# Kernel tuning notes

Measured on AMD Instinct MI355X. Metric: run time of the kernel, lower is better.

## Reference

```python
import jax, jax.numpy as jnp
import numpy as np

B, T, N, P2, K_S = 8, 64, 128, 256, 64

def setup_inputs() -> dict:
    key = jax.random.key(0)
    k1, k2, k3, k4 = jax.random.split(key, 4)
    x = jax.random.normal(k1, (B, T, N, P2), dtype=jnp.float32)
    W_Q = jax.random.uniform(k2, (P2, K_S), dtype=jnp.float32)
    W_K = jax.random.uniform(k3, (P2, K_S), dtype=jnp.float32)
    W_V = jax.random.uniform(k4, (P2, P2), dtype=jnp.float32)
    return {"x": x, "W_Q": W_Q, "W_K": W_K, "W_V": W_V}

def reference(x, W_Q, W_K, W_V):
    # x: [B, T, N, P2]
    q = jnp.einsum('btnp,pk->btnk', x, W_Q)          # [B,T,N,K_S]
    k = jnp.einsum('btnp,pk->btnk', x, W_K)          # [B,T,N,K_S]
    v = jnp.einsum('btnp,pq->btnq', x, W_V)          # [B,T,N,P2]
    scale = jnp.sqrt(jnp.asarray(K_S, dtype=x.dtype))
    scores = jnp.einsum('btik,btjk->btij', q, k) / scale  # [B,T,N,N]
    # NOTE: original uses nn.Softmax(dim=1) -> softmax over the T axis.
    attn = jax.nn.softmax(scores, axis=1)
    return jnp.einsum('btij,btjq->btiq', attn, v)    # [B,T,N,P2]
```

## Files before the change

kernel.cpp:

```cpp
#include <hip/hip_runtime.h>
#include <hip/hip_bf16.h>

#define Bv 8
#define Tv 64
#define Nv 128
#define P2v 256
#define KSv 64

typedef __attribute__((ext_vector_type(8))) short bf8;
typedef __attribute__((ext_vector_type(4))) float f4;

#define MFMA16(a, b, c) __builtin_amdgcn_mfma_f32_16x16x32_bf16((a), (b), (c), 0, 0, 0)

__device__ __forceinline__ unsigned short f2bf(float f) {
  unsigned u = __float_as_uint(f);
  return (unsigned short)((u + 0x7fffu + ((u >> 16) & 1u)) >> 16);
}
__device__ __forceinline__ float bf2f(unsigned short h) {
  return __uint_as_float(((unsigned)h) << 16);
}

__device__ __forceinline__ int swz64(int r, int c) {
  return r * 64 + ((((c >> 3)) ^ (r & 7)) << 3) + (c & 7);
}
__device__ __forceinline__ int swz32(int r, int c) {
  return r * 32 + ((((c >> 3)) ^ (r & 3)) << 3) + (c & 7);
}
__device__ __forceinline__ int swz128(int r, int c) {
  return r * 128 + ((((c >> 3)) ^ (r & 7)) << 3) + (c & 7);
}

__global__ __launch_bounds__(256) void prep_w_kernel(
    const float* __restrict__ Wq, const float* __restrict__ Wk,
    const float* __restrict__ Wv, unsigned short* __restrict__ wqh,
    unsigned short* __restrict__ wql, unsigned short* __restrict__ wkh,
    unsigned short* __restrict__ wkl, unsigned short* __restrict__ wvf) {
  const int e = blockIdx.x * 256 + threadIdx.x;
  if (e < 32768) {
    const float* W = (e < 16384) ? Wq : Wk;
    unsigned short* oh = (e < 16384) ? wqh : wkh;
    unsigned short* ol = (e < 16384) ? wql : wkl;
    const int t = e & 16383;
    const int jj = t & 7, lane = (t >> 3) & 63, nt = (t >> 9) & 3, pt = t >> 11;
    const int p = pt * 32 + 8 * (lane >> 4) + jj;
    const int n = nt * 16 + (lane & 15);
    const float v = W[p * KSv + n];
    const unsigned short h = f2bf(v);
    oh[t] = h;
    ol[t] = f2bf(v - bf2f(h));
  } else {
    const int t = e - 32768;
    const int jj = t & 7, lane = (t >> 3) & 63, nt = (t >> 9) & 15, pt = t >> 13;
    const int p = pt * 32 + 8 * (lane >> 4) + jj;
    const int q = nt * 16 + (lane & 15);
    wvf[t] = f2bf(Wv[p * P2v + q]);
  }
}

__global__ __launch_bounds__(512) void qk_kernel(
    const float* __restrict__ x, const unsigned short* __restrict__ wqh,
    const unsigned short* __restrict__ wql,
    const unsigned short* __restrict__ wkh,
    const unsigned short* __restrict__ wkl, float* __restrict__ S,
    unsigned short* __restrict__ Xh) {
  __shared__ alignas(16) unsigned short xh_l[Nv * 32];
  __shared__ alignas(16) unsigned short xl_l[Nv * 32];
  __shared__ alignas(16) unsigned short qh_l[Nv * KSv];
  __shared__ alignas(16) unsigned short ql_l[Nv * KSv];
  __shared__ alignas(16) unsigned short kh_l[Nv * KSv];
  __shared__ alignas(16) unsigned short kl_l[Nv * KSv];
  const int bt = blockIdx.x;
  const float* __restrict__ X = x + (size_t)bt * (Nv * P2v);
  const int tid = threadIdx.x, lane = tid & 63, wid = tid >> 6;
  const int lg = lane >> 4, lr = lane & 15;
  const bool isQ = (wid < 4);
  const int nt = wid & 3;
  const unsigned short* __restrict__ wh = isQ ? wqh : wkh;
  const unsigned short* __restrict__ wl = isQ ? wql : wkl;

  const f4 zero = {0.f, 0.f, 0.f, 0.f};
  f4 acc[8];
#pragma unroll
  for (int rt = 0; rt < 8; ++rt) acc[rt] = zero;

  const int srow = tid >> 2;
  const int sp = (tid & 3) * 8;
  const float* __restrict__ Xrow = X + srow * P2v + sp;
  unsigned short* __restrict__ XhRow =
      Xh ? (Xh + (size_t)(bt * Nv + srow) * P2v + sp) : (unsigned short*)0;

  float4 pv0 = *(const float4*)(Xrow);
  float4 pv1 = *(const float4*)(Xrow + 4);
  bf8 pwh = *(const bf8*)(wh + (nt * 64 + lane) * 8);
  bf8 pwl = *(const bf8*)(wl + (nt * 64 + lane) * 8);

  for (int c = 0; c < 8; ++c) {
    ushort4 h0, l0, h1, l1;
    h0.x = f2bf(pv0.x); l0.x = f2bf(pv0.x - bf2f(h0.x));
    h0.y = f2bf(pv0.y); l0.y = f2bf(pv0.y - bf2f(h0.y));
    h0.z = f2bf(pv0.z); l0.z = f2bf(pv0.z - bf2f(h0.z));
    h0.w = f2bf(pv0.w); l0.w = f2bf(pv0.w - bf2f(h0.w));
    h1.x = f2bf(pv1.x); l1.x = f2bf(pv1.x - bf2f(h1.x));
    h1.y = f2bf(pv1.y); l1.y = f2bf(pv1.y - bf2f(h1.y));
    h1.z = f2bf(pv1.z); l1.z = f2bf(pv1.z - bf2f(h1.z));
    h1.w = f2bf(pv1.w); l1.w = f2bf(pv1.w - bf2f(h1.w));
    const bf8 cwh = pwh, cwl = pwl;

    if (XhRow) {
      *(ushort4*)(XhRow + c * 32) = h0;
      *(ushort4*)(XhRow + c * 32 + 4) = h1;
    }

    __syncthreads();
    const int off = swz32(srow, sp);
    *(ushort4*)(xh_l + off) = h0;
    *(ushort4*)(xh_l + off + 4) = h1;
    *(ushort4*)(xl_l + off) = l0;
    *(ushort4*)(xl_l + off + 4) = l1;

    if (c < 7) {
      pv0 = *(const float4*)(Xrow + (c + 1) * 32);
      pv1 = *(const float4*)(Xrow + (c + 1) * 32 + 4);
      const int wo = (((c + 1) * 4 + nt) * 64 + lane) * 8;
      pwh = *(const bf8*)(wh + wo);
      pwl = *(const bf8*)(wl + wo);
    }
    __syncthreads();
#pragma unroll
    for (int rt = 0; rt < 8; ++rt) {
      const int xoff = swz32(rt * 16 + lr, lg * 8);
      const bf8 xh = *(const bf8*)(xh_l + xoff);
      const bf8 xl = *(const bf8*)(xl_l + xoff);
      acc[rt] = MFMA16(xh, cwh, acc[rt]);
      acc[rt] = MFMA16(xh, cwl, acc[rt]);
      acc[rt] = MFMA16(xl, cwh, acc[rt]);
    }
  }

  unsigned short* const oh = isQ ? qh_l : kh_l;
  unsigned short* const ol = isQ ? ql_l : kl_l;
#pragma unroll
  for (int rt = 0; rt < 8; ++rt) {
#pragma unroll
    for (int rr = 0; rr < 4; ++rr) {
      const int i = rt * 16 + 4 * lg + rr;
      const int ks = nt * 16 + lr;
      const int off = swz64(i, ks);
      const float v = acc[rt][rr];
      const unsigned short h = f2bf(v);
      oh[off] = h;
      ol[off] = f2bf(v - bf2f(h));
    }
  }
  __syncthreads();

  const int r0 = wid * 16;
  f4 aS[8];
#pragma unroll
  for (int n = 0; n < 8; ++n) aS[n] = zero;
#pragma unroll
  for (int kt2 = 0; kt2 < 2; ++kt2) {
    const int qoff = swz64(r0 + lr, kt2 * 32 + lg * 8);
    const bf8 fqh = *(const bf8*)(qh_l + qoff);
    const bf8 fql = *(const bf8*)(ql_l + qoff);
#pragma unroll
    for (int n = 0; n < 8; ++n) {
      const int koff = swz64(n * 16 + lr, kt2 * 32 + lg * 8);
      const bf8 fkh = *(const bf8*)(kh_l + koff);
      const bf8 fkl = *(const bf8*)(kl_l + koff);
      aS[n] = MFMA16(fqh, fkh, aS[n]);
      aS[n] = MFMA16(fqh, fkl, aS[n]);
      aS[n] = MFMA16(fql, fkh, aS[n]);
    }
  }
  float* __restrict__ Sb = S + (size_t)bt * (Nv * Nv);
#pragma unroll
  for (int n = 0; n < 8; ++n) {
#pragma unroll
    for (int rr = 0; rr < 4; ++rr) {
      Sb[(r0 + 4 * lg + rr) * Nv + n * 16 + lr] = aS[n][rr] * 0.125f;
    }
  }
}

__global__ __launch_bounds__(256) void softmax_t_kernel(
    const float* __restrict__ S, unsigned short* __restrict__ Abf) {
  const int idx = blockIdx.x * 256 + threadIdx.x;
  const int j = idx & (Nv - 1);
  const int i = (idx >> 7) & (Nv - 1);
  const int b = idx >> 14;
  const size_t base = ((size_t)b * Tv * Nv * Nv) + (size_t)i * Nv + j;

  float vals[Tv];
  float m = -1e30f;
#pragma unroll
  for (int t = 0; t < Tv; ++t) {
    const float v = S[base + (size_t)t * Nv * Nv];
    vals[t] = v;
    m = fmaxf(m, v);
  }
  float s = 0.f;
#pragma unroll
  for (int t = 0; t < Tv; ++t) {
    const float e = __expf(vals[t] - m);
    vals[t] = e;
    s += e;
  }
  const float inv = 1.f / s;
#pragma unroll
  for (int t = 0; t < Tv; ++t) {
    Abf[base + (size_t)t * Nv * Nv] = f2bf(vals[t] * inv);
  }
}

__global__ __launch_bounds__(512) void av_direct_kernel(
    const unsigned short* __restrict__ Xh,
    const unsigned short* __restrict__ wvf,
    const unsigned short* __restrict__ Abf, float* __restrict__ out) {
  __shared__ alignas(16) unsigned short vth[Nv * Nv];
  const int bt = blockIdx.x;
  const unsigned short* __restrict__ Xb = Xh + (size_t)bt * (Nv * P2v);
  const unsigned short* __restrict__ Ab = Abf + (size_t)bt * (Nv * Nv);
  float* __restrict__ ob = out + (size_t)bt * (Nv * P2v);
  const int tid = threadIdx.x, lane = tid & 63, wid = tid >> 6;
  const int lg = lane >> 4, lr = lane & 15;
  const int r0 = wid * 16;

  const f4 zero = {0.f, 0.f, 0.f, 0.f};
  f4 aV[16];
#pragma unroll
  for (int n = 0; n < 16; ++n) aV[n] = zero;

#pragma unroll
  for (int kt = 0; kt < 8; ++kt) {
    const bf8 fv0 = *(const bf8*)(wvf + ((kt * 16 + wid) * 64 + lane) * 8);
    const bf8 fv1 = *(const bf8*)(wvf + ((kt * 16 + 8 + wid) * 64 + lane) * 8);
#pragma unroll
    for (int rt = 0; rt < 8; ++rt) {
      const bf8 xf = *(const bf8*)(Xb + (rt * 16 + lr) * P2v + kt * 32 + lg * 8);
      aV[rt] = MFMA16(xf, fv0, aV[rt]);
      aV[8 + rt] = MFMA16(xf, fv1, aV[8 + rt]);
    }
  }

  bf8 af[4];
#pragma unroll
  for (int kt = 0; kt < 4; ++kt) {
    af[kt] = *(const bf8*)(Ab + (r0 + lr) * Nv + kt * 32 + lg * 8);
  }

#pragma unroll
  for (int h = 0; h < 2; ++h) {
    if (h == 1) __syncthreads();
    const int ql = wid * 16 + lr;
#pragma unroll
    for (int rt = 0; rt < 8; ++rt) {
      const int j0 = rt * 16 + 4 * lg;
      ushort4 pk;
      pk.x = f2bf(aV[h * 8 + rt][0]);
      pk.y = f2bf(aV[h * 8 + rt][1]);
      pk.z = f2bf(aV[h * 8 + rt][2]);
      pk.w = f2bf(aV[h * 8 + rt][3]);
      *(ushort4*)(vth + swz128(ql, j0)) = pk;
    }
    __syncthreads();

    f4 aO[8];
#pragma unroll
    for (int n = 0; n < 8; ++n) aO[n] = zero;
#pragma unroll
    for (int kt = 0; kt < 4; ++kt) {
#pragma unroll
      for (int n = 0; n < 8; ++n) {
        const bf8 vf =
            *(const bf8*)(vth + swz128(n * 16 + lr, kt * 32 + lg * 8));
        aO[n] = MFMA16(af[kt], vf, aO[n]);
      }
    }
#pragma unroll
    for (int n = 0; n < 8; ++n) {
#pragma unroll
      for (int rr = 0; rr < 4; ++rr) {
        ob[(r0 + 4 * lg + rr) * P2v + h * 128 + n * 16 + lr] = aO[n][rr];
      }
    }
  }
}

__global__ __launch_bounds__(512) void av_kernel(
    const float* __restrict__ x, const unsigned short* __restrict__ wvf,
    const unsigned short* __restrict__ Abf, float* __restrict__ out) {
  __shared__ alignas(16) unsigned short xa[Nv * KSv];
  __shared__ alignas(16) unsigned short vth[Nv * Nv];
  const int bt = blockIdx.x;
  const float* __restrict__ X = x + (size_t)bt * (Nv * P2v);
  const unsigned short* __restrict__ Ab = Abf + (size_t)bt * (Nv * Nv);
  float* __restrict__ ob = out + (size_t)bt * (Nv * P2v);
  const int tid = threadIdx.x, lane = tid & 63, wid = tid >> 6;
  const int lg = lane >> 4, lr = lane & 15;
  const int r0 = wid * 16;

  bf8 af[4];
#pragma unroll
  for (int kt = 0; kt < 4; ++kt) {
    af[kt] = *(const bf8*)(Ab + (r0 + lr) * Nv + kt * 32 + lg * 8);
  }

  const f4 zero = {0.f, 0.f, 0.f, 0.f};
  f4 aV[16];
#pragma unroll
  for (int n = 0; n < 16; ++n) aV[n] = zero;

  const int srow = tid >> 4;
  const int sp = (tid & 15) * 4;
  const float* __restrict__ Xrow = X + srow * P2v + sp;

  float4 pf0 = *(const float4*)(Xrow);
  float4 pf1 = *(const float4*)(Xrow + 32 * P2v);
  float4 pf2 = *(const float4*)(Xrow + 64 * P2v);
  float4 pf3 = *(const float4*)(Xrow + 96 * P2v);

  for (int c = 0; c < 4; ++c) {
    ushort4 q0, q1, q2, q3;
    q0.x = f2bf(pf0.x); q0.y = f2bf(pf0.y); q0.z = f2bf(pf0.z); q0.w = f2bf(pf0.w);
    q1.x = f2bf(pf1.x); q1.y = f2bf(pf1.y); q1.z = f2bf(pf1.z); q1.w = f2bf(pf1.w);
    q2.x = f2bf(pf2.x); q2.y = f2bf(pf2.y); q2.z = f2bf(pf2.z); q2.w = f2bf(pf2.w);
    q3.x = f2bf(pf3.x); q3.y = f2bf(pf3.y); q3.z = f2bf(pf3.z); q3.w = f2bf(pf3.w);

    __syncthreads();
    *(ushort4*)(xa + swz64(srow, sp)) = q0;
    *(ushort4*)(xa + swz64(srow + 32, sp)) = q1;
    *(ushort4*)(xa + swz64(srow + 64, sp)) = q2;
    *(ushort4*)(xa + swz64(srow + 96, sp)) = q3;

    if (c < 3) {
      pf0 = *(const float4*)(Xrow + (c + 1) * 64);
      pf1 = *(const float4*)(Xrow + (c + 1) * 64 + 32 * P2v);
      pf2 = *(const float4*)(Xrow + (c + 1) * 64 + 64 * P2v);
      pf3 = *(const float4*)(Xrow + (c + 1) * 64 + 96 * P2v);
    }
    __syncthreads();
#pragma unroll
    for (int ktl = 0; ktl < 2; ++ktl) {
      const int kt = c * 2 + ktl;
#pragma unroll
      for (int h = 0; h < 2; ++h) {
        const int ntile = h * 8 + wid;
        const int o = ((kt * 16 + ntile) * 64 + lane) * 8;
        const bf8 fv = *(const bf8*)(wvf + o);
#pragma unroll
        for (int rt = 0; rt < 8; ++rt) {
          const bf8 xh =
              *(const bf8*)(xa + swz64(rt * 16 + lr, ktl * 32 + lg * 8));
          aV[h * 8 + rt] = MFMA16(xh, fv, aV[h * 8 + rt]);
        }
      }
    }
  }

#pragma unroll
  for (int h = 0; h < 2; ++h) {
    if (h == 1) __syncthreads();
    const int ql = wid * 16 + lr;
#pragma unroll
    for (int rt = 0; rt < 8; ++rt) {
      const int j0 = rt * 16 + 4 * lg;
      ushort4 pk;
      pk.x = f2bf(aV[h * 8 + rt][0]);
      pk.y = f2bf(aV[h * 8 + rt][1]);
      pk.z = f2bf(aV[h * 8 + rt][2]);
      pk.w = f2bf(aV[h * 8 + rt][3]);
      *(ushort4*)(vth + swz128(ql, j0)) = pk;
    }
    __syncthreads();

    f4 aO[8];
#pragma unroll
    for (int n = 0; n < 8; ++n) aO[n] = zero;
#pragma unroll
    for (int kt = 0; kt < 4; ++kt) {
#pragma unroll
      for (int n = 0; n < 8; ++n) {
        const bf8 vf =
            *(const bf8*)(vth + swz128(n * 16 + lr, kt * 32 + lg * 8));
        aO[n] = MFMA16(af[kt], vf, aO[n]);
      }
    }
#pragma unroll
    for (int n = 0; n < 8; ++n) {
#pragma unroll
      for (int rr = 0; rr < 4; ++rr) {
        ob[(r0 + 4 * lg + rr) * P2v + h * 128 + n * 16 + lr] = aO[n][rr];
      }
    }
  }
}

extern "C" void kernel_launch(void* const* d_in, const int* in_sizes, int n_in,
                              void* d_out, int out_size, void* d_ws,
                              size_t ws_size, hipStream_t stream) {
  const float* x = (const float*)d_in[0];
  const float* Wq = (const float*)d_in[1];
  const float* Wk = (const float*)d_in[2];
  const float* Wv = (const float*)d_in[3];
  float* out = (float*)d_out;

  unsigned short* wqh = (unsigned short*)d_ws;
  unsigned short* wql = wqh + 16384;
  unsigned short* wkh = wql + 16384;
  unsigned short* wkl = wkh + 16384;
  unsigned short* wvf = wkl + 16384;
  float* S = (float*)((char*)d_ws + 262144);
  unsigned short* Abf = (unsigned short*)((char*)d_ws + 262144 + 33554432);
  unsigned short* Xh =
      (unsigned short*)((char*)d_ws + 262144 + 33554432 + 16777216);
  const size_t need_big = 262144ull + 33554432ull + 16777216ull + 33554432ull;
  const bool big = (ws_size >= need_big);

  hipLaunchKernelGGL(prep_w_kernel, dim3(384), dim3(256), 0, stream, Wq, Wk,
                     Wv, wqh, wql, wkh, wkl, wvf);
  hipLaunchKernelGGL(qk_kernel, dim3(Bv * Tv), dim3(512), 0, stream, x, wqh,
                     wql, wkh, wkl, S, big ? Xh : (unsigned short*)0);
  hipLaunchKernelGGL(softmax_t_kernel, dim3(Bv * Nv * Nv / 256), dim3(256), 0,
                     stream, S, Abf);
  if (big) {
    hipLaunchKernelGGL(av_direct_kernel, dim3(Bv * Tv), dim3(512), 0, stream,
                       Xh, wvf, Abf, out);
  } else {
    hipLaunchKernelGGL(av_kernel, dim3(Bv * Tv), dim3(512), 0, stream, x, wvf,
                       Abf, out);
  }
}
```

Before: 97.32 us.

## Alias LDS buffers, stage X through LDS in AV kernel, vectorize score/output stores

The QK kernel now aliases its x-staging and q/k LDS buffers into a single array, which lowers LDS use per block and may allow higher occupancy. The S and output stores are vectorized to float4 by swapping the MFMA operands so each lane holds contiguous columns. The direct AV kernel now stages bf16 X tiles in swizzled LDS with register prefetch instead of reading fragments straight from global memory. The V^T buffer is split into two 64-column swizzled halves. These changes add extra barriers and depend on the aliasing being safe after the added sync.

After: 82.17 us. -15.6%, faster.

```diff
diff --git a/kernel.cpp b/kernel.cpp
--- a/kernel.cpp
+++ b/kernel.cpp
@@ -25,9 +25,6 @@
 }
 __device__ __forceinline__ int swz32(int r, int c) {
   return r * 32 + ((((c >> 3)) ^ (r & 3)) << 3) + (c & 7);
-}
-__device__ __forceinline__ int swz128(int r, int c) {
-  return r * 128 + ((((c >> 3)) ^ (r & 7)) << 3) + (c & 7);
 }
 
 __global__ __launch_bounds__(256) void prep_w_kernel(
@@ -63,12 +60,13 @@
     const unsigned short* __restrict__ wkh,
     const unsigned short* __restrict__ wkl, float* __restrict__ S,
     unsigned short* __restrict__ Xh) {
-  __shared__ alignas(16) unsigned short xh_l[Nv * 32];
-  __shared__ alignas(16) unsigned short xl_l[Nv * 32];
-  __shared__ alignas(16) unsigned short qh_l[Nv * KSv];
-  __shared__ alignas(16) unsigned short ql_l[Nv * KSv];
-  __shared__ alignas(16) unsigned short kh_l[Nv * KSv];
-  __shared__ alignas(16) unsigned short kl_l[Nv * KSv];
+  __shared__ alignas(16) unsigned short sh[4 * Nv * KSv];
+  unsigned short* const xh_l = sh;
+  unsigned short* const xl_l = sh + Nv * 32;
+  unsigned short* const qh_l = sh;
+  unsigned short* const ql_l = sh + 8192;
+  unsigned short* const kh_l = sh + 16384;
+  unsigned short* const kl_l = sh + 24576;
   const int bt = blockIdx.x;
   const float* __restrict__ X = x + (size_t)bt * (Nv * P2v);
   const int tid = threadIdx.x, lane = tid & 63, wid = tid >> 6;
@@ -137,6 +135,8 @@
     }
   }
 
+  __syncthreads();
+
   unsigned short* const oh = isQ ? qh_l : kh_l;
   unsigned short* const ol = isQ ? ql_l : kl_l;
 #pragma unroll
@@ -168,18 +168,20 @@
       const int koff = swz64(n * 16 + lr, kt2 * 32 + lg * 8);
       const bf8 fkh = *(const bf8*)(kh_l + koff);
       const bf8 fkl = *(const bf8*)(kl_l + koff);
-      aS[n] = MFMA16(fqh, fkh, aS[n]);
-      aS[n] = MFMA16(fqh, fkl, aS[n]);
-      aS[n] = MFMA16(fql, fkh, aS[n]);
+      aS[n] = MFMA16(fkh, fqh, aS[n]);
+      aS[n] = MFMA16(fkl, fqh, aS[n]);
+      aS[n] = MFMA16(fkh, fql, aS[n]);
     }
   }
   float* __restrict__ Sb = S + (size_t)bt * (Nv * Nv);
 #pragma unroll
   for (int n = 0; n < 8; ++n) {
-#pragma unroll
-    for (int rr = 0; rr < 4; ++rr) {
-      Sb[(r0 + 4 * lg + rr) * Nv + n * 16 + lr] = aS[n][rr] * 0.125f;
-    }
+    float4 v;
+    v.x = aS[n][0] * 0.125f;
+    v.y = aS[n][1] * 0.125f;
+    v.z = aS[n][2] * 0.125f;
+    v.w = aS[n][3] * 0.125f;
+    *(float4*)(Sb + (r0 + lr) * Nv + n * 16 + 4 * lg) = v;
   }
 }
 
@@ -213,11 +215,13 @@
   }
 }
 
-__global__ __launch_bounds__(512) void av_direct_kernel(
+__global__ __launch_bounds__(512) void av_kernel(
     const unsigned short* __restrict__ Xh,
     const unsigned short* __restrict__ wvf,
     const unsigned short* __restrict__ Abf, float* __restrict__ out) {
-  __shared__ alignas(16) unsigned short vth[Nv * Nv];
+  __shared__ alignas(16) unsigned short xa[Nv * KSv];
+  __shared__ alignas(16) unsigned short vthA[Nv * KSv];
+  __shared__ alignas(16) unsigned short vthB[Nv * KSv];
   const int bt = blockIdx.x;
   const unsigned short* __restrict__ Xb = Xh + (size_t)bt * (Nv * P2v);
   const unsigned short* __restrict__ Ab = Abf + (size_t)bt * (Nv * Nv);
@@ -231,15 +235,38 @@
 #pragma unroll
   for (int n = 0; n < 16; ++n) aV[n] = zero;
 
-#pragma unroll
-  for (int kt = 0; kt < 8; ++kt) {
-    const bf8 fv0 = *(const bf8*)(wvf + ((kt * 16 + wid) * 64 + lane) * 8);
-    const bf8 fv1 = *(const bf8*)(wvf + ((kt * 16 + 8 + wid) * 64 + lane) * 8);
-#pragma unroll
-    for (int rt = 0; rt < 8; ++rt) {
-      const bf8 xf = *(const bf8*)(Xb + (rt * 16 + lr) * P2v + kt * 32 + lg * 8);
-      aV[rt] = MFMA16(xf, fv0, aV[rt]);
-      aV[8 + rt] = MFMA16(xf, fv1, aV[8 + rt]);
+  const int srow2 = tid >> 3;
+  const int sp8 = (tid & 7) * 8;
+  const unsigned short* __restrict__ Xrow2 = Xb + srow2 * P2v + sp8;
+
+  uint4 pg0 = *(const uint4*)(Xrow2);
+  uint4 pg1 = *(const uint4*)(Xrow2 + 64 * P2v);
+
+  for (int c = 0; c < 4; ++c) {
+    __syncthreads();
+    *(uint4*)(xa + swz64(srow2, sp8)) = pg0;
+    *(uint4*)(xa + swz64(srow2 + 64, sp8)) = pg1;
+
+    if (c < 3) {
+      pg0 = *(const uint4*)(Xrow2 + (c + 1) * 64);
+      pg1 = *(const uint4*)(Xrow2 + (c + 1) * 64 + 64 * P2v);
+    }
+    __syncthreads();
+#pragma unroll
+    for (int ktl = 0; ktl < 2; ++ktl) {
+      const int kt = c * 2 + ktl;
+#pragma unroll
+      for (int h = 0; h < 2; ++h) {
+        const int ntile = h * 8 + wid;
+        const int o = ((kt * 16 + ntile) * 64 + lane) * 8;
+        const bf8 fv = *(const bf8*)(wvf + o);
+#pragma unroll
+        for (int rt = 0; rt < 8; ++rt) {
+          const bf8 xh =
+              *(const bf8*)(xa + swz64(rt * 16 + lr, ktl * 32 + lg * 8));
+          aV[h * 8 + rt] = MFMA16(xh, fv, aV[h * 8 + rt]);
+        }
+      }
     }
   }
 
@@ -261,7 +288,11 @@
       pk.y = f2bf(aV[h * 8 + rt][1]);
       pk.z = f2bf(aV[h * 8 + rt][2]);
       pk.w = f2bf(aV[h * 8 + rt][3]);
-      *(ushort4*)(vth + swz128(ql, j0)) = pk;
+      if (rt < 4) {
+        *(ushort4*)(vthA + swz64(ql, j0)) = pk;
+      } else {
+        *(ushort4*)(vthB + swz64(ql, j0 - 64)) = pk;
+      }
     }
     __syncthreads();
 
@@ -272,26 +303,30 @@
     for (int kt = 0; kt < 4; ++kt) {
 #pragma unroll
       for (int n = 0; n < 8; ++n) {
-        const bf8 vf =
-            *(const bf8*)(vth + swz128(n * 16 + lr, kt * 32 + lg * 8));
-        aO[n] = MFMA16(af[kt], vf, aO[n]);
+        const unsigned short* vsrc = (kt < 2) ? vthA : vthB;
+        const int col = (kt & 1) * 32 + lg * 8;
+        const bf8 vf = *(const bf8*)(vsrc + swz64(n * 16 + lr, col));
+        aO[n] = MFMA16(vf, af[kt], aO[n]);
       }
     }
 #pragma unroll
     for (int n = 0; n < 8; ++n) {
-#pragma unroll
-      for (int rr = 0; rr < 4; ++rr) {
-        ob[(r0 + 4 * lg + rr) * P2v + h * 128 + n * 16 + lr] = aO[n][rr];
-      }
-    }
-  }
-}
-
-__global__ __launch_bounds__(512) void av_kernel(
+      float4 v;
+      v.x = aO[n][0];
+      v.y = aO[n][1];
+      v.z = aO[n][2];
+      v.w = aO[n][3];
+      *(float4*)(ob + (r0 + lr) * P2v + h * 128 + n * 16 + 4 * lg) = v;
+    }
+  }
+}
+
+__global__ __launch_bounds__(512) void av_fb_kernel(
     const float* __restrict__ x, const unsigned short* __restrict__ wvf,
     const unsigned short* __restrict__ Abf, float* __restrict__ out) {
   __shared__ alignas(16) unsigned short xa[Nv * KSv];
-  __shared__ alignas(16) unsigned short vth[Nv * Nv];
+  __shared__ alignas(16) unsigned short vthA[Nv * KSv];
+  __shared__ alignas(16) unsigned short vthB[Nv * KSv];
   const int bt = blockIdx.x;
   const float* __restrict__ X = x + (size_t)bt * (Nv * P2v);
   const unsigned short* __restrict__ Ab = Abf + (size_t)bt * (Nv * Nv);
@@ -300,12 +335,6 @@
   const int lg = lane >> 4, lr = lane & 15;
   const int r0 = wid * 16;
 
-  bf8 af[4];
-#pragma unroll
-  for (int kt = 0; kt < 4; ++kt) {
-    af[kt] = *(const bf8*)(Ab + (r0 + lr) * Nv + kt * 32 + lg * 8);
-  }
-
   const f4 zero = {0.f, 0.f, 0.f, 0.f};
   f4 aV[16];
 #pragma unroll
@@ -356,6 +385,12 @@
         }
       }
     }
+  }
+
+  bf8 af[4];
+#pragma unroll
+  for (int kt = 0; kt < 4; ++kt) {
+    af[kt] = *(const bf8*)(Ab + (r0 + lr) * Nv + kt * 32 + lg * 8);
   }
 
 #pragma unroll
@@ -370,7 +405,11 @@
       pk.y = f2bf(aV[h * 8 + rt][1]);
       pk.z = f2bf(aV[h * 8 + rt][2]);
       pk.w = f2bf(aV[h * 8 + rt][3]);
-      *(ushort4*)(vth + swz128(ql, j0)) = pk;
+      if (rt < 4) {
+        *(ushort4*)(vthA + swz64(ql, j0)) = pk;
+      } else {
+        *(ushort4*)(vthB + swz64(ql, j0 - 64)) = pk;
+      }
     }
     __syncthreads();
 
@@ -381,17 +420,20 @@
     for (int kt = 0; kt < 4; ++kt) {
 #pragma unroll
       for (int n = 0; n < 8; ++n) {
-        const bf8 vf =
-            *(const bf8*)(vth + swz128(n * 16 + lr, kt * 32 + lg * 8));
-        aO[n] = MFMA16(af[kt], vf, aO[n]);
+        const unsigned short* vsrc = (kt < 2) ? vthA : vthB;
+        const int col = (kt & 1) * 32 + lg * 8;
+        const bf8 vf = *(const bf8*)(vsrc + swz64(n * 16 + lr, col));
+        aO[n] = MFMA16(vf, af[kt], aO[n]);
       }
     }
 #pragma unroll
     for (int n = 0; n < 8; ++n) {
-#pragma unroll
-      for (int rr = 0; rr < 4; ++rr) {
-        ob[(r0 + 4 * lg + rr) * P2v + h * 128 + n * 16 + lr] = aO[n][rr];
-      }
+      float4 v;
+      v.x = aO[n][0];
+      v.y = aO[n][1];
+      v.z = aO[n][2];
+      v.w = aO[n][3];
+      *(float4*)(ob + (r0 + lr) * P2v + h * 128 + n * 16 + 4 * lg) = v;
     }
   }
 }
@@ -424,10 +466,10 @@
   hipLaunchKernelGGL(softmax_t_kernel, dim3(Bv * Nv * Nv / 256), dim3(256), 0,
                      stream, S, Abf);
   if (big) {
-    hipLaunchKernelGGL(av_direct_kernel, dim3(Bv * Tv), dim3(512), 0, stream,
-                       Xh, wvf, Abf, out);
+    hipLaunchKernelGGL(av_kernel, dim3(Bv * Tv), dim3(512), 0, stream, Xh, wvf,
+                       Abf, out);
   } else {
-    hipLaunchKernelGGL(av_kernel, dim3(Bv * Tv), dim3(512), 0, stream, x, wvf,
-                       Abf, out);
-  }
-}
+    hipLaunchKernelGGL(av_fb_kernel, dim3(Bv * Tv), dim3(512), 0, stream, x,
+                       wvf, Abf, out);
+  }
+}
```
